# Optimization experiments

Hardware: AMD Instinct MI355X
Metric: run time of the kernel (lower is better)

Reference implementation:

```python
import jax, jax.numpy as jnp
import numpy as np

B = 1_000_000
FEAT = 64
EMBEDDING_SIZE = 128


def setup_inputs() -> dict:
    key = jax.random.key(0)
    k0, k1, k2 = jax.random.split(key, 3)
    x = jax.random.normal(k0, (B, FEAT), dtype=jnp.float32)
    W1 = jax.random.normal(k1, (FEAT, FEAT), dtype=jnp.float32) * (1.0 / np.sqrt(FEAT))
    b1 = jnp.zeros((FEAT,), dtype=jnp.float32)
    W2 = jax.random.normal(k2, (FEAT, EMBEDDING_SIZE), dtype=jnp.float32) * (1.0 / np.sqrt(FEAT))
    b2 = jnp.zeros((EMBEDDING_SIZE,), dtype=jnp.float32)
    return {"x": x, "W1": W1, "b1": b1, "W2": W2, "b2": b2}


def reference(x, W1, b1, W2, b2):
    # head: Linear(64,64) -> ReLU -> Linear(64, EMBEDDING_SIZE)
    h = jax.nn.relu(x @ W1 + b1)
    e = h @ W2 + b2
    # per-sample L2 normalize with zero-norm guard (Normalize module)
    norm = jnp.linalg.norm(e, axis=-1, keepdims=True)  # [B,1]
    out = jnp.where(norm == 0, jnp.zeros_like(e), e / jnp.where(norm == 0, 1.0, norm))
    return out
```

## Files before the change

kernel.cpp:

```cpp
#include <hip/hip_runtime.h>
#include <stdint.h>


typedef __attribute__((ext_vector_type(8))) short short8;
typedef __attribute__((ext_vector_type(4))) float f32x4;

__device__ __forceinline__ ushort f2bf(float f) {
    union { float f; uint32_t u; } v; v.f = f;
    uint32_t u = v.u;
    u += 0x7fffu + ((u >> 16) & 1u);
    return (ushort)(u >> 16);
}
__device__ __forceinline__ uint32_t pack2(float a, float b) {
    return (uint32_t)f2bf(a) | ((uint32_t)f2bf(b) << 16);
}

__global__ __launch_bounds__(256)
void fused_head_kernel(const float* __restrict__ x,
                       const float* __restrict__ W1,
                       const float* __restrict__ b1,
                       const float* __restrict__ W2,
                       const float* __restrict__ b2,
                       float* __restrict__ out,
                       int ntiles)
{
    __shared__ ushort w1t[64][72];
    __shared__ ushort w2t[128][72];
    __shared__ ushort htile[4][16][72];
    __shared__ __align__(16) float b1s[64];
    __shared__ __align__(16) float b2s[128];

    const int tid  = threadIdx.x;
    const int wave = tid >> 6;
    const int lane = tid & 63;
    const int l16  = lane & 15;
    const int lq   = lane >> 4;

    int tile = blockIdx.x;

    f32x4 uA[4], uB[4];
    {
        const float* p = x + ((size_t)(tile * 64 + wave * 16 + l16)) * 64 + lq * 8;
        uA[0] = *(const f32x4*)p;        uA[1] = *(const f32x4*)(p + 4);
        uA[2] = *(const f32x4*)(p + 32); uA[3] = *(const f32x4*)(p + 36);
    }

    for (int idx = tid; idx < 64 * 64; idx += 256) {
        int k = idx >> 6, n = idx & 63;
        w1t[n][k] = f2bf(W1[idx]);
    }
    for (int idx = tid; idx < 64 * 128; idx += 256) {
        int k = idx >> 7, n = idx & 127;
        w2t[n][k] = f2bf(W2[idx]);
    }
    if (tid < 64)  b1s[tid] = b1[tid];
    if (tid < 128) b2s[tid] = b2[tid];
    __syncthreads();

    auto loadx = [&](f32x4* u, int t) {
        const float* p = x + ((size_t)(t * 64 + wave * 16 + l16)) * 64 + lq * 8;
        u[0] = *(const f32x4*)p;        u[1] = *(const f32x4*)(p + 4);
        u[2] = *(const f32x4*)(p + 32); u[3] = *(const f32x4*)(p + 36);
    };

    auto process = [&](const f32x4* u, int t) {
        short8 xf[2];
#pragma unroll
        for (int h = 0; h < 2; ++h) {
            short8 v;
            v[0] = (short)f2bf(u[2*h][0]);   v[1] = (short)f2bf(u[2*h][1]);
            v[2] = (short)f2bf(u[2*h][2]);   v[3] = (short)f2bf(u[2*h][3]);
            v[4] = (short)f2bf(u[2*h+1][0]); v[5] = (short)f2bf(u[2*h+1][1]);
            v[6] = (short)f2bf(u[2*h+1][2]); v[7] = (short)f2bf(u[2*h+1][3]);
            xf[h] = v;
        }

        f32x4 acc1[4] = {};
#pragma unroll
        for (int h = 0; h < 2; ++h)
#pragma unroll
            for (int nt = 0; nt < 4; ++nt) {
                short8 wf = *(const short8*)&w1t[nt * 16 + l16][h * 32 + lq * 8];
                acc1[nt] = __builtin_amdgcn_mfma_f32_16x16x32_bf16(wf, xf[h], acc1[nt], 0, 0, 0);
            }

#pragma unroll
        for (int nt = 0; nt < 4; ++nt) {
            f32x4 bv = *(const f32x4*)&b1s[nt * 16 + lq * 4];
            float h0 = acc1[nt][0] + bv[0]; h0 = h0 > 0.f ? h0 : 0.f;
            float h1 = acc1[nt][1] + bv[1]; h1 = h1 > 0.f ? h1 : 0.f;
            float h2 = acc1[nt][2] + bv[2]; h2 = h2 > 0.f ? h2 : 0.f;
            float h3 = acc1[nt][3] + bv[3]; h3 = h3 > 0.f ? h3 : 0.f;
            uint32_t* dst = (uint32_t*)&htile[wave][l16][nt * 16 + lq * 4];
            dst[0] = pack2(h0, h1);
            dst[1] = pack2(h2, h3);
        }

        f32x4 acc2[8] = {};
#pragma unroll
        for (int h = 0; h < 2; ++h) {
            short8 hf = *(const short8*)&htile[wave][l16][h * 32 + lq * 8];
#pragma unroll
            for (int nt = 0; nt < 8; ++nt) {
                short8 wf = *(const short8*)&w2t[nt * 16 + l16][h * 32 + lq * 8];
                acc2[nt] = __builtin_amdgcn_mfma_f32_16x16x32_bf16(wf, hf, acc2[nt], 0, 0, 0);
            }
        }

        float ss = 0.f;
#pragma unroll
        for (int nt = 0; nt < 8; ++nt) {
            f32x4 bv = *(const f32x4*)&b2s[nt * 16 + lq * 4];
#pragma unroll
            for (int r = 0; r < 4; ++r) {
                float e = acc2[nt][r] + bv[r];
                acc2[nt][r] = e;
                ss += e * e;
            }
        }
        ss += __shfl_xor(ss, 16, 64);
        ss += __shfl_xor(ss, 32, 64);
        float sc = ss > 0.f ? rsqrtf(ss) : 0.f;

        float* po = out + ((size_t)(t * 64 + wave * 16 + l16)) * 128 + lq * 4;
#pragma unroll
        for (int nt = 0; nt < 8; ++nt) {
            f32x4 v;
            v[0] = acc2[nt][0] * sc; v[1] = acc2[nt][1] * sc;
            v[2] = acc2[nt][2] * sc; v[3] = acc2[nt][3] * sc;
            *(f32x4*)(po + nt * 16) = v;
        }
    };

    int next = tile + gridDim.x;
    while (true) {
        bool hasB = next < ntiles;
        if (hasB) loadx(uB, next);
        process(uA, tile);
        if (!hasB) break;
        tile = next; next += gridDim.x;
        bool hasA = next < ntiles;
        if (hasA) loadx(uA, next);
        process(uB, tile);
        if (!hasA) break;
        tile = next; next += gridDim.x;
    }
}

extern "C" void kernel_launch(void* const* d_in, const int* in_sizes, int n_in,
                              void* d_out, int out_size, void* d_ws, size_t ws_size,
                              hipStream_t stream) {
    const float* x  = (const float*)d_in[0];
    const float* W1 = (const float*)d_in[1];
    const float* b1 = (const float*)d_in[2];
    const float* W2 = (const float*)d_in[3];
    const float* b2 = (const float*)d_in[4];
    float* out = (float*)d_out;

    const int nrows  = in_sizes[0] / 64;
    const int ntiles = nrows / 64;
    int grid = ntiles < 3125 ? ntiles : 3125;

    hipLaunchKernelGGL(fused_head_kernel, dim3(grid), dim3(256), 0, stream,
                       x, W1, b1, W2, b2, out, ntiles);
}
```

Baseline: 700.5 us.

## Assign contiguous tile chunks per block with register prefetch and nontemporal stores

Replaces the grid-stride loop with double-buffered register sets by a fixed chunk of 5 contiguous tiles per block. The next tile's x is loaded into the same registers right after they are converted to bf16, which reduces register use. Output writes become nontemporal stores so they do not pollute the cache. The grid stays the same size (3125 blocks for 15625 tiles), but the prefetch depth and the access pattern change, and the in-loop prefetch now sits before the MFMA work.

```diff
diff --git a/kernel.cpp b/kernel.cpp
--- a/kernel.cpp
+++ b/kernel.cpp
@@ -4,6 +4,8 @@
 
 typedef __attribute__((ext_vector_type(8))) short short8;
 typedef __attribute__((ext_vector_type(4))) float f32x4;
+
+#define TILES_PER_BLOCK 5
 
 __device__ __forceinline__ ushort f2bf(float f) {
     union { float f; uint32_t u; } v; v.f = f;
@@ -36,14 +38,15 @@
     const int l16  = lane & 15;
     const int lq   = lane >> 4;
 
-    int tile = blockIdx.x;
+    const int t0   = blockIdx.x * TILES_PER_BLOCK;
+    if (t0 >= ntiles) return;
+    const int tcnt = (ntiles - t0 < TILES_PER_BLOCK) ? (ntiles - t0) : TILES_PER_BLOCK;
 
-    f32x4 uA[4], uB[4];
-    {
-        const float* p = x + ((size_t)(tile * 64 + wave * 16 + l16)) * 64 + lq * 8;
-        uA[0] = *(const f32x4*)p;        uA[1] = *(const f32x4*)(p + 4);
-        uA[2] = *(const f32x4*)(p + 32); uA[3] = *(const f32x4*)(p + 36);
-    }
+    const float* px = x + ((size_t)(t0 * 64 + wave * 16 + l16)) * 64 + lq * 8;
+
+    f32x4 u[4];
+    u[0] = *(const f32x4*)px;        u[1] = *(const f32x4*)(px + 4);
+    u[2] = *(const f32x4*)(px + 32); u[3] = *(const f32x4*)(px + 36);
 
     for (int idx = tid; idx < 64 * 64; idx += 256) {
         int k = idx >> 6, n = idx & 63;
@@ -57,13 +60,9 @@
     if (tid < 128) b2s[tid] = b2[tid];
     __syncthreads();
 
-    auto loadx = [&](f32x4* u, int t) {
-        const float* p = x + ((size_t)(t * 64 + wave * 16 + l16)) * 64 + lq * 8;
-        u[0] = *(const f32x4*)p;        u[1] = *(const f32x4*)(p + 4);
-        u[2] = *(const f32x4*)(p + 32); u[3] = *(const f32x4*)(p + 36);
-    };
+    for (int i = 0; i < tcnt; ++i) {
+        const int t = t0 + i;
 
-    auto process = [&](const f32x4* u, int t) {
         short8 xf[2];
 #pragma unroll
         for (int h = 0; h < 2; ++h) {
@@ -73,6 +72,12 @@
             v[4] = (short)f2bf(u[2*h+1][0]); v[5] = (short)f2bf(u[2*h+1][1]);
             v[6] = (short)f2bf(u[2*h+1][2]); v[7] = (short)f2bf(u[2*h+1][3]);
             xf[h] = v;
+        }
+
+        if (i + 1 < tcnt) {
+            const float* p = px + (size_t)(i + 1) * 4096;
+            u[0] = *(const f32x4*)p;        u[1] = *(const f32x4*)(p + 4);
+            u[2] = *(const f32x4*)(p + 32); u[3] = *(const f32x4*)(p + 36);
         }
 
         f32x4 acc1[4] = {};
@@ -128,22 +133,8 @@
             f32x4 v;
             v[0] = acc2[nt][0] * sc; v[1] = acc2[nt][1] * sc;
             v[2] = acc2[nt][2] * sc; v[3] = acc2[nt][3] * sc;
-            *(f32x4*)(po + nt * 16) = v;
+            __builtin_nontemporal_store(v, (f32x4*)(po + nt * 16));
         }
-    };
-
-    int next = tile + gridDim.x;
-    while (true) {
-        bool hasB = next < ntiles;
-        if (hasB) loadx(uB, next);
-        process(uA, tile);
-        if (!hasB) break;
-        tile = next; next += gridDim.x;
-        bool hasA = next < ntiles;
-        if (hasA) loadx(uA, next);
-        process(uB, tile);
-        if (!hasA) break;
-        tile = next; next += gridDim.x;
     }
 }
 
@@ -159,7 +150,7 @@
 
     const int nrows  = in_sizes[0] / 64;
     const int ntiles = nrows / 64;
-    int grid = ntiles < 3125 ? ntiles : 3125;
+    const int grid   = (ntiles + TILES_PER_BLOCK - 1) / TILES_PER_BLOCK;
 
     hipLaunchKernelGGL(fused_head_kernel, dim3(grid), dim3(256), 0, stream,
                        x, W1, b1, W2, b2, out, ntiles);
```

Measured after the change: 717.0 us. 1.02x slower.
